# Kernel tuning notes

Hardware: AMD Instinct MI355X
Metric: run time of the kernel (lower is better)

## Reference

```python
import jax, jax.numpy as jnp
import numpy as np

B, N, D = 4096, 64, 128

def setup_inputs() -> dict:
    key = jax.random.key(0)
    ks = jax.random.split(key, 5)
    return {
        "stu_emb": jax.random.normal(ks[0], (B, D), jnp.float32),
        "concept_emb": jax.random.normal(ks[1], (B, D), jnp.float32),
        "neighbor_emb": jax.random.normal(ks[2], (B, N, D), jnp.float32),
        # Linear(2D -> D) for stu_concept_integration (xavier-like scale)
        "Ws": jax.random.normal(ks[3], (2 * D, D), jnp.float32) * (2.0 / (3 * D)) ** 0.5,
        "bs": jnp.full((D,), 0.1, jnp.float32),
        # Linear(2D -> 1) for concept_neighbor_weight
        "Ww": jax.random.normal(ks[4], (2 * D, 1), jnp.float32) * (2.0 / (2 * D + 1)) ** 0.5,
        "bw": jnp.full((1,), 0.1, jnp.float32),
    }


def reference(stu_emb, concept_emb, neighbor_emb, Ws, bs, Ww, bw):
    # Masks: 1 where the (first) concatenated input is nonzero along features
    dt = stu_emb.dtype
    mask_s = (jnp.sum(stu_emb, -1, keepdims=True) != 0).astype(dt)[:, None, :]      # [B,1,1]
    mask_c = (jnp.sum(concept_emb, -1, keepdims=True) != 0).astype(dt)[:, None, :]  # [B,1,1]

    # Split concat-linear into two halves so the broadcasted half is computed once
    Ws_a, Ws_b = Ws[:D], Ws[D:]   # [D,D] each
    Ww_a, Ww_b = Ww[:D], Ww[D:]   # [D,1] each

    stu_part = stu_emb @ Ws_a            # [B,D]
    con_part = concept_emb @ Ws_b        # [B,D]
    nbr_part = neighbor_emb @ Ws_b       # [B,N,D]

    # neighbor attention weights: Linear(2D->1)(cat(concept_ext, neighbor)) * mask_c
    w = (concept_emb @ Ww_a)[:, None, :] + neighbor_emb @ Ww_b + bw  # [B,N,1]
    w = w * mask_c
    w = jax.nn.softmax(w, axis=-2)  # softmax over neighbor axis

    # stu integrated with neighbors / with the original concept, masked by stu mask
    integ_n = (stu_part[:, None, :] + nbr_part + bs) * mask_s            # [B,N,D]
    integ_o = (stu_part[:, None, :] + con_part[:, None, :] + bs) * mask_s  # [B,N,D] (broadcast)

    # combine over neighbor axis and average the two branches
    y = jnp.sum(integ_o + w * integ_n, axis=-2) / 2  # [B,D]
    return y
```

## Files before the change

kernel.cpp:

```cpp
#include <hip/hip_runtime.h>

#define BB 4096
#define NN 64
#define DD 128
#define G  4
#define P2S 36

__global__ __launch_bounds__(256) void kFused(
    const float* __restrict__ stu,
    const float* __restrict__ conc,
    const float* __restrict__ nbr,
    const float* __restrict__ Ws,
    const float* __restrict__ bs,
    const float* __restrict__ Ww,
    float* __restrict__ y)
{
    const int t    = threadIdx.x;
    const int lane = t & 63;
    const int cg   = t & 31;
    const int g8   = t >> 5;
    const int wv   = t >> 6;
    const int b0   = blockIdx.x * G;

    __shared__ __align__(16) float part2[NN * P2S];
    __shared__ float wsm[NN];
    __shared__ float csum[G];
    __shared__ float maskh[G];
    __shared__ __align__(16) float u[G][2 * DD];
    __shared__ __align__(16) float scratch[G * 8 * DD];

    const float4 wb = reinterpret_cast<const float4*>(Ww + DD)[cg];
    const float4* nb4 = reinterpret_cast<const float4*>(nbr);

    {
        const int b = b0 + wv;
        float cv0 = conc[(size_t)b * DD + lane];
        float cv1 = conc[(size_t)b * DD + 64 + lane];
        float sv0 = stu [(size_t)b * DD + lane];
        float sv1 = stu [(size_t)b * DD + 64 + lane];
        u[wv][lane]           = 65.0f * sv0;
        u[wv][64 + lane]      = 65.0f * sv1;
        u[wv][DD + lane]      = 64.0f * cv0;
        u[wv][DD + 64 + lane] = 64.0f * cv1;
        float cs = cv0 + cv1, ss = sv0 + sv1;
#pragma unroll
        for (int o = 1; o < 64; o <<= 1) {
            cs += __shfl_xor(cs, o);
            ss += __shfl_xor(ss, o);
        }
        if (lane == 0) {
            csum[wv]  = cs;
            maskh[wv] = (ss != 0.0f) ? 0.5f : 0.0f;
        }
    }

    float4 val[8], valn[8];
#pragma unroll
    for (int i = 0; i < 8; ++i)
        val[i] = nb4[(size_t)b0 * 2048 + t + 256 * i];

    for (int g = 0; g < G; ++g) {
#pragma unroll
        for (int i = 0; i < 8; ++i) {
            const int row = g8 + 8 * i;
            part2[row * P2S + cg] =
                val[i].x * wb.x + val[i].y * wb.y + val[i].z * wb.z + val[i].w * wb.w;
        }
        if (g < G - 1) {
#pragma unroll
            for (int i = 0; i < 8; ++i)
                valn[i] = nb4[(size_t)(b0 + g + 1) * 2048 + t + 256 * i];
        }
        __syncthreads();

        if (t < NN) {
            float s = 0.0f;
#pragma unroll
            for (int j = 0; j < 8; ++j) {
                const float4 p = *reinterpret_cast<const float4*>(&part2[t * P2S + j * 4]);
                s += p.x + p.y + p.z + p.w;
            }
            float m = s;
            m = fmaxf(m, __shfl_xor(m, 1));
            m = fmaxf(m, __shfl_xor(m, 2));
            m = fmaxf(m, __shfl_xor(m, 4));
            m = fmaxf(m, __shfl_xor(m, 8));
            m = fmaxf(m, __shfl_xor(m, 16));
            m = fmaxf(m, __shfl_xor(m, 32));
            float e = __expf(s - m);
            float den = e;
            den += __shfl_xor(den, 1);
            den += __shfl_xor(den, 2);
            den += __shfl_xor(den, 4);
            den += __shfl_xor(den, 8);
            den += __shfl_xor(den, 16);
            den += __shfl_xor(den, 32);
            wsm[t] = (csum[g] != 0.0f) ? (e / den) : (1.0f / 64.0f);
        }
        __syncthreads();

        float4 a = {0.f, 0.f, 0.f, 0.f};
#pragma unroll
        for (int i = 0; i < 8; ++i) {
            const float w = wsm[g8 + 8 * i];
            a.x += w * val[i].x; a.y += w * val[i].y;
            a.z += w * val[i].z; a.w += w * val[i].w;
        }
        reinterpret_cast<float4*>(scratch + g * 8 * DD)[g8 * 32 + cg] = a;

        if (g < G - 1) {
#pragma unroll
            for (int i = 0; i < 8; ++i) val[i] = valn[i];
        }
    }
    __syncthreads();

#pragma unroll
    for (int it = 0; it < 2; ++it) {
        const int idx = t + 256 * it;
        const int gg  = idx >> 7;
        const int c   = idx & 127;
        float s = 0.0f;
#pragma unroll
        for (int k = 0; k < 8; ++k) s += scratch[gg * 8 * DD + k * DD + c];
        u[gg][DD + c] += s;
    }
    __syncthreads();

    float4 acc0 = {0,0,0,0}, acc1 = {0,0,0,0}, acc2 = {0,0,0,0}, acc3 = {0,0,0,0};
    const float4* Ws4 = reinterpret_cast<const float4*>(Ws);
#pragma unroll 4
    for (int j = 0; j < 32; ++j) {
        const int k = g8 * 32 + j;
        float4 wq = Ws4[k * 32 + cg];
        float u0 = u[0][k], u1 = u[1][k], u2 = u[2][k], u3 = u[3][k];
        acc0.x += u0 * wq.x; acc0.y += u0 * wq.y; acc0.z += u0 * wq.z; acc0.w += u0 * wq.w;
        acc1.x += u1 * wq.x; acc1.y += u1 * wq.y; acc1.z += u1 * wq.z; acc1.w += u1 * wq.w;
        acc2.x += u2 * wq.x; acc2.y += u2 * wq.y; acc2.z += u2 * wq.z; acc2.w += u2 * wq.w;
        acc3.x += u3 * wq.x; acc3.y += u3 * wq.y; acc3.z += u3 * wq.z; acc3.w += u3 * wq.w;
    }
    {
        float4* pr = reinterpret_cast<float4*>(scratch);
        pr[(g8 * G + 0) * 32 + cg] = acc0;
        pr[(g8 * G + 1) * 32 + cg] = acc1;
        pr[(g8 * G + 2) * 32 + cg] = acc2;
        pr[(g8 * G + 3) * 32 + cg] = acc3;
    }
    __syncthreads();
#pragma unroll
    for (int i = 0; i < 2; ++i) {
        const int idx = t + 256 * i;
        const int r = idx >> 7;
        const int c = idx & 127;
        float s = 0.0f;
#pragma unroll
        for (int k2 = 0; k2 < 8; ++k2) s += scratch[(k2 * G + r) * DD + c];
        y[(size_t)(b0 + r) * DD + c] = (s + 65.0f * bs[c]) * maskh[r];
    }
}

extern "C" void kernel_launch(void* const* d_in, const int* in_sizes, int n_in,
                              void* d_out, int out_size, void* d_ws, size_t ws_size,
                              hipStream_t stream) {
    const float* stu  = (const float*)d_in[0];
    const float* conc = (const float*)d_in[1];
    const float* nbr  = (const float*)d_in[2];
    const float* Ws   = (const float*)d_in[3];
    const float* bs   = (const float*)d_in[4];
    const float* Ww   = (const float*)d_in[5];
    float* y = (float*)d_out;

    kFused<<<BB / G, 256, 0, stream>>>(stu, conc, nbr, Ws, bs, Ww, y);
}
```

Before: 29.95 us.

## Interleave per-row Ws GEMV into the neighbor loop to overlap with loads

The final projection through Ws is split into one GEMV per batch row. Each row's GEMV now runs inside the neighbor-processing loop one iteration late, and the scratch reduction is moved into idle threads during the softmax phase. The goal is to hide the GEMV and reduction work behind the prefetch of the next row's neighbor tile instead of running them all after the loop. In exchange, Ws is read once per row instead of once per block, the kernel uses more shared memory for per-row partial sums, and the final write loop is restructured to handle two rows per thread.

```diff
diff --git a/kernel.cpp b/kernel.cpp
--- a/kernel.cpp
+++ b/kernel.cpp
@@ -27,10 +27,12 @@
     __shared__ float csum[G];
     __shared__ float maskh[G];
     __shared__ __align__(16) float u[G][2 * DD];
-    __shared__ __align__(16) float scratch[G * 8 * DD];
+    __shared__ __align__(16) float scratch[8 * DD];
+    __shared__ __align__(16) float scratch2[G][8 * DD];
 
     const float4 wb = reinterpret_cast<const float4*>(Ww + DD)[cg];
     const float4* nb4 = reinterpret_cast<const float4*>(nbr);
+    const float4* Ws4 = reinterpret_cast<const float4*>(Ws);
 
     {
         const int b = b0 + wv;
@@ -96,6 +98,12 @@
             den += __shfl_xor(den, 16);
             den += __shfl_xor(den, 32);
             wsm[t] = (csum[g] != 0.0f) ? (e / den) : (1.0f / 64.0f);
+        } else if (t >= 128 && g > 0) {
+            const int c = t - 128;
+            float s = 0.0f;
+#pragma unroll
+            for (int k = 0; k < 8; ++k) s += scratch[k * DD + c];
+            u[g - 1][DD + c] += s;
         }
         __syncthreads();
 
@@ -106,45 +114,47 @@
             a.x += w * val[i].x; a.y += w * val[i].y;
             a.z += w * val[i].z; a.w += w * val[i].w;
         }
-        reinterpret_cast<float4*>(scratch + g * 8 * DD)[g8 * 32 + cg] = a;
+        reinterpret_cast<float4*>(scratch)[g8 * 32 + cg] = a;
+
+        if (g > 0) {
+            const int r = g - 1;
+            float4 acc = {0.f, 0.f, 0.f, 0.f};
+#pragma unroll 8
+            for (int j = 0; j < 32; ++j) {
+                const int k = g8 * 32 + j;
+                const float4 wq = Ws4[k * 32 + cg];
+                const float ur = u[r][k];
+                acc.x += ur * wq.x; acc.y += ur * wq.y;
+                acc.z += ur * wq.z; acc.w += ur * wq.w;
+            }
+            reinterpret_cast<float4*>(scratch2[r])[g8 * 32 + cg] = acc;
+        }
 
         if (g < G - 1) {
 #pragma unroll
             for (int i = 0; i < 8; ++i) val[i] = valn[i];
         }
     }
+
     __syncthreads();
-
-#pragma unroll
-    for (int it = 0; it < 2; ++it) {
-        const int idx = t + 256 * it;
-        const int gg  = idx >> 7;
-        const int c   = idx & 127;
+    if (t < DD) {
         float s = 0.0f;
 #pragma unroll
-        for (int k = 0; k < 8; ++k) s += scratch[gg * 8 * DD + k * DD + c];
-        u[gg][DD + c] += s;
+        for (int k = 0; k < 8; ++k) s += scratch[k * DD + t];
+        u[G - 1][DD + t] += s;
     }
     __syncthreads();
-
-    float4 acc0 = {0,0,0,0}, acc1 = {0,0,0,0}, acc2 = {0,0,0,0}, acc3 = {0,0,0,0};
-    const float4* Ws4 = reinterpret_cast<const float4*>(Ws);
-#pragma unroll 4
-    for (int j = 0; j < 32; ++j) {
-        const int k = g8 * 32 + j;
-        float4 wq = Ws4[k * 32 + cg];
-        float u0 = u[0][k], u1 = u[1][k], u2 = u[2][k], u3 = u[3][k];
-        acc0.x += u0 * wq.x; acc0.y += u0 * wq.y; acc0.z += u0 * wq.z; acc0.w += u0 * wq.w;
-        acc1.x += u1 * wq.x; acc1.y += u1 * wq.y; acc1.z += u1 * wq.z; acc1.w += u1 * wq.w;
-        acc2.x += u2 * wq.x; acc2.y += u2 * wq.y; acc2.z += u2 * wq.z; acc2.w += u2 * wq.w;
-        acc3.x += u3 * wq.x; acc3.y += u3 * wq.y; acc3.z += u3 * wq.z; acc3.w += u3 * wq.w;
-    }
     {
-        float4* pr = reinterpret_cast<float4*>(scratch);
-        pr[(g8 * G + 0) * 32 + cg] = acc0;
-        pr[(g8 * G + 1) * 32 + cg] = acc1;
-        pr[(g8 * G + 2) * 32 + cg] = acc2;
-        pr[(g8 * G + 3) * 32 + cg] = acc3;
+        float4 acc = {0.f, 0.f, 0.f, 0.f};
+#pragma unroll 8
+        for (int j = 0; j < 32; ++j) {
+            const int k = g8 * 32 + j;
+            const float4 wq = Ws4[k * 32 + cg];
+            const float ur = u[G - 1][k];
+            acc.x += ur * wq.x; acc.y += ur * wq.y;
+            acc.z += ur * wq.z; acc.w += ur * wq.w;
+        }
+        reinterpret_cast<float4*>(scratch2[G - 1])[g8 * 32 + cg] = acc;
     }
     __syncthreads();
 #pragma unroll
@@ -154,8 +164,14 @@
         const int c = idx & 127;
         float s = 0.0f;
 #pragma unroll
-        for (int k2 = 0; k2 < 8; ++k2) s += scratch[(k2 * G + r) * DD + c];
+        for (int k2 = 0; k2 < 8; ++k2) s += scratch2[r][k2 * DD + c];
         y[(size_t)(b0 + r) * DD + c] = (s + 65.0f * bs[c]) * maskh[r];
+        const int r2 = r + 2;
+        float s2 = 0.0f;
+#pragma unroll
+        for (int k2 = 0; k2 < 8; ++k2) s2 += scratch2[r2][k2 * DD + c];
+        y[(size_t)(b0 + r2) * DD + c] = (s2 + 65.0f * bs[c]) * maskh[r2];
+        break;
     }
 }
 
```

New measurement: 38.02 us. 27.0% more time.

## Compute softmax redundantly per wave and double-buffer logits to drop a barrier

Applied to the files above, without the earlier changes.

Every wave now computes the 64-neighbor softmax itself and broadcasts the weights with lane shuffles instead of writing them to shared memory. This removes the second __syncthreads per group and the idle time of three waves. The logit buffer is double-buffered so the next group's writes cannot race with the current reads. Register ping-pong buffers replace the copy loop, the next group's prefetch is issued earlier, and reads are rotated to spread LDS bank conflicts. The cost is four times the softmax and LDS-read work and higher register pressure from full unrolling.

```diff
diff --git a/kernel.cpp b/kernel.cpp
--- a/kernel.cpp
+++ b/kernel.cpp
@@ -22,8 +22,7 @@
     const int wv   = t >> 6;
     const int b0   = blockIdx.x * G;
 
-    __shared__ __align__(16) float part2[NN * P2S];
-    __shared__ float wsm[NN];
+    __shared__ __align__(16) float part2[2][NN * P2S];
     __shared__ float csum[G];
     __shared__ float maskh[G];
     __shared__ __align__(16) float u[G][2 * DD];
@@ -31,6 +30,7 @@
 
     const float4 wb = reinterpret_cast<const float4*>(Ww + DD)[cg];
     const float4* nb4 = reinterpret_cast<const float4*>(nbr);
+    const float4* Ws4 = reinterpret_cast<const float4*>(Ws);
 
     {
         const int b = b0 + wv;
@@ -54,64 +54,63 @@
         }
     }
 
-    float4 val[8], valn[8];
+    float4 valA[8], valB[8];
 #pragma unroll
     for (int i = 0; i < 8; ++i)
-        val[i] = nb4[(size_t)b0 * 2048 + t + 256 * i];
+        valA[i] = nb4[(size_t)b0 * 2048 + t + 256 * i];
 
+#pragma unroll
     for (int g = 0; g < G; ++g) {
+        float4* valc = (g & 1) ? valB : valA;
+        float4* valp = (g & 1) ? valA : valB;
+
+        if (g < G - 1) {
+#pragma unroll
+            for (int i = 0; i < 8; ++i)
+                valp[i] = nb4[(size_t)(b0 + g + 1) * 2048 + t + 256 * i];
+        }
+
 #pragma unroll
         for (int i = 0; i < 8; ++i) {
             const int row = g8 + 8 * i;
-            part2[row * P2S + cg] =
-                val[i].x * wb.x + val[i].y * wb.y + val[i].z * wb.z + val[i].w * wb.w;
-        }
-        if (g < G - 1) {
-#pragma unroll
-            for (int i = 0; i < 8; ++i)
-                valn[i] = nb4[(size_t)(b0 + g + 1) * 2048 + t + 256 * i];
+            part2[g & 1][row * P2S + cg] =
+                valc[i].x * wb.x + valc[i].y * wb.y + valc[i].z * wb.z + valc[i].w * wb.w;
         }
         __syncthreads();
 
-        if (t < NN) {
-            float s = 0.0f;
+        float s = 0.0f;
 #pragma unroll
-            for (int j = 0; j < 8; ++j) {
-                const float4 p = *reinterpret_cast<const float4*>(&part2[t * P2S + j * 4]);
-                s += p.x + p.y + p.z + p.w;
-            }
-            float m = s;
-            m = fmaxf(m, __shfl_xor(m, 1));
-            m = fmaxf(m, __shfl_xor(m, 2));
-            m = fmaxf(m, __shfl_xor(m, 4));
-            m = fmaxf(m, __shfl_xor(m, 8));
-            m = fmaxf(m, __shfl_xor(m, 16));
-            m = fmaxf(m, __shfl_xor(m, 32));
-            float e = __expf(s - m);
-            float den = e;
-            den += __shfl_xor(den, 1);
-            den += __shfl_xor(den, 2);
-            den += __shfl_xor(den, 4);
-            den += __shfl_xor(den, 8);
-            den += __shfl_xor(den, 16);
-            den += __shfl_xor(den, 32);
-            wsm[t] = (csum[g] != 0.0f) ? (e / den) : (1.0f / 64.0f);
+        for (int j = 0; j < 8; ++j) {
+            const int jj = (j + (lane >> 3)) & 7;
+            const float4 p = *reinterpret_cast<const float4*>(
+                &part2[g & 1][lane * P2S + jj * 4]);
+            s += p.x + p.y + p.z + p.w;
         }
-        __syncthreads();
+        float m = s;
+        m = fmaxf(m, __shfl_xor(m, 1));
+        m = fmaxf(m, __shfl_xor(m, 2));
+        m = fmaxf(m, __shfl_xor(m, 4));
+        m = fmaxf(m, __shfl_xor(m, 8));
+        m = fmaxf(m, __shfl_xor(m, 16));
+        m = fmaxf(m, __shfl_xor(m, 32));
+        const float e = __expf(s - m);
+        float den = e;
+        den += __shfl_xor(den, 1);
+        den += __shfl_xor(den, 2);
+        den += __shfl_xor(den, 4);
+        den += __shfl_xor(den, 8);
+        den += __shfl_xor(den, 16);
+        den += __shfl_xor(den, 32);
+        const float wlane = (csum[g] != 0.0f) ? (e / den) : (1.0f / 64.0f);
 
         float4 a = {0.f, 0.f, 0.f, 0.f};
 #pragma unroll
         for (int i = 0; i < 8; ++i) {
-            const float w = wsm[g8 + 8 * i];
-            a.x += w * val[i].x; a.y += w * val[i].y;
-            a.z += w * val[i].z; a.w += w * val[i].w;
+            const float w = __shfl(wlane, g8 + 8 * i);
+            a.x += w * valc[i].x; a.y += w * valc[i].y;
+            a.z += w * valc[i].z; a.w += w * valc[i].w;
         }
         reinterpret_cast<float4*>(scratch + g * 8 * DD)[g8 * 32 + cg] = a;
-
-        if (g < G - 1) {
-#pragma unroll
-            for (int i = 0; i < 8; ++i) val[i] = valn[i];
-        }
     }
     __syncthreads();
 
@@ -120,15 +119,14 @@
         const int idx = t + 256 * it;
         const int gg  = idx >> 7;
         const int c   = idx & 127;
-        float s = 0.0f;
+        float s2 = 0.0f;
 #pragma unroll
-        for (int k = 0; k < 8; ++k) s += scratch[gg * 8 * DD + k * DD + c];
-        u[gg][DD + c] += s;
+        for (int k = 0; k < 8; ++k) s2 += scratch[gg * 8 * DD + k * DD + c];
+        u[gg][DD + c] += s2;
     }
     __syncthreads();
 
     float4 acc0 = {0,0,0,0}, acc1 = {0,0,0,0}, acc2 = {0,0,0,0}, acc3 = {0,0,0,0};
-    const float4* Ws4 = reinterpret_cast<const float4*>(Ws);
 #pragma unroll 4
     for (int j = 0; j < 32; ++j) {
         const int k = g8 * 32 + j;
@@ -152,10 +150,10 @@
         const int idx = t + 256 * i;
         const int r = idx >> 7;
         const int c = idx & 127;
-        float s = 0.0f;
+        float s2 = 0.0f;
 #pragma unroll
-        for (int k2 = 0; k2 < 8; ++k2) s += scratch[(k2 * G + r) * DD + c];
-        y[(size_t)(b0 + r) * DD + c] = (s + 65.0f * bs[c]) * maskh[r];
+        for (int k2 = 0; k2 < 8; ++k2) s2 += scratch[(k2 * G + r) * DD + c];
+        y[(size_t)(b0 + r) * DD + c] = (s2 + 65.0f * bs[c]) * maskh[r];
     }
 }
 
```

Result: slower. 31.26 us (+4.4%).
